# Kernel optimization log

Hardware: AMD Instinct MI355X
Metric: run time of the kernel (lower is better)

## Reference

```python
import jax, jax.numpy as jnp
import numpy as np

SEG = 4      # segment_size
H = 8        # n_heads
D = 1024     # d_model
B = 8
S = 4096


def setup_inputs() -> dict:
    key = jax.random.key(0)
    ks = jax.random.split(key, 9)
    s = 0.02  # init scale for weights
    return {
        "x": jax.random.normal(ks[0], (B, S, D), dtype=jnp.float32),
        "proj_qk_w": jax.random.normal(ks[1], (D, D), dtype=jnp.float32) * s,
        "proj_qk_b": jax.random.normal(ks[2], (D,), dtype=jnp.float32) * s,
        "proj_v_w": jax.random.normal(ks[3], (D, D), dtype=jnp.float32) * s,
        "proj_v_b": jax.random.normal(ks[4], (D,), dtype=jnp.float32) * s,
        "in_proj_w": jax.random.normal(ks[5], (3 * D, D), dtype=jnp.float32) * s,
        "in_proj_b": jax.random.normal(ks[6], (3 * D,), dtype=jnp.float32) * s,
        "out_proj_w": jax.random.normal(ks[7], (D, D), dtype=jnp.float32) * s,
        "out_proj_b": jax.random.normal(ks[8], (D,), dtype=jnp.float32) * s,
    }


def reference(x, proj_qk_w, proj_qk_b, proj_v_w, proj_v_b,
              in_proj_w, in_proj_b, out_proj_w, out_proj_b):
    b, seq_len, d = x.shape
    hd = d // H
    # torch: pad = seg - S % seg  (pads a full segment when S % seg == 0)
    pad = SEG - seq_len % SEG
    x = jnp.concatenate([x, x[:, :pad]], axis=1)          # [b, T, d]
    T = seq_len + pad
    a = T // SEG
    # cat(chunk(x, a, dim=1), dim=0): block-major stacking -> [a*b, SEG, d]
    xb = x.reshape(b, a, SEG, d).transpose(1, 0, 2, 3).reshape(a * b, SEG, d)

    # extra projections (same qk projection used for query and key)
    qk_in = xb @ proj_qk_w.T + proj_qk_b                   # [a*b, SEG, d]
    v_in = xb @ proj_v_w.T + proj_v_b

    # nn.MultiheadAttention in-projection
    wq, wk, wv = jnp.split(in_proj_w, 3, axis=0)
    bq, bk, bv = jnp.split(in_proj_b, 3)
    q = (qk_in @ wq.T + bq).reshape(a * b, SEG, H, hd)
    k = (qk_in @ wk.T + bk).reshape(a * b, SEG, H, hd)
    v = (v_in @ wv.T + bv).reshape(a * b, SEG, H, hd)

    scale = 1.0 / np.sqrt(hd).astype(np.float32)
    scores = jnp.einsum('nqhd,nkhd->nhqk', q * scale, k)   # [a*b, H, SEG, SEG]
    # diagonal exclusion mask (True on the diagonal = masked)
    diag = jnp.eye(SEG, dtype=bool)
    scores = jnp.where(diag[None, None], jnp.finfo(scores.dtype).min, scores)
    attn = jax.nn.softmax(scores, axis=-1)
    o = jnp.einsum('nhqk,nkhd->nqhd', attn, v).reshape(a * b, SEG, d)
    o = o @ out_proj_w.T + out_proj_b                      # [a*b, SEG, d]

    # cat(chunk(x, a, dim=0), dim=1): invert the block stacking
    out = o.reshape(a, b, SEG, d).transpose(1, 0, 2, 3).reshape(b, T, d)
    return out[:, :seq_len]
```

## Files before the change

### kernel.cpp

```cpp
#include <hip/hip_runtime.h>
#include <hip/hip_bf16.h>

typedef __bf16 bf16x8 __attribute__((ext_vector_type(8)));
typedef float f32x4 __attribute__((ext_vector_type(4)));

__device__ __forceinline__ float bf2f(unsigned int u) {
    unsigned int x = u << 16;
    return __builtin_bit_cast(float, x);
}
__device__ __forceinline__ unsigned short f2bf(float f) {
    unsigned int x = __builtin_bit_cast(unsigned int, f);
    x += 0x7fffu + ((x >> 16) & 1u);
    return (unsigned short)(x >> 16);
}

__device__ __forceinline__ void gld_lds16(const unsigned short* g, unsigned short* s) {
    __builtin_amdgcn_global_load_lds((const __attribute__((address_space(1))) void*)g,
                                     (__attribute__((address_space(3))) void*)s, 16, 0, 0);
}

template<bool OUT_F32>
__global__ __launch_bounds__(256) void gemm_bt(
    const unsigned short* __restrict__ A, int lda,
    const unsigned short* __restrict__ B,
    const unsigned short* __restrict__ B2, long bsplit,
    const float* __restrict__ bias,
    void* __restrict__ C, int N, int K)
{
    __shared__ unsigned short As[128 * 32];
    __shared__ unsigned short Bs[128 * 32];
    const int tid   = threadIdx.x;
    const int lane  = tid & 63;
    const int wave  = tid >> 6;
    const int wm    = (wave >> 1) * 64;
    const int wn    = (wave & 1) * 64;
    const int lrow  = lane & 15;
    const int lquad = lane >> 4;
    const long bm = (long)blockIdx.y * 128;
    const long bn = (long)blockIdx.x * 128;
    const unsigned short* Bp = (bm >= bsplit) ? B2 : B;

    f32x4 acc[4][4];
#pragma unroll
    for (int i = 0; i < 4; i++)
#pragma unroll
        for (int j = 0; j < 4; j++)
            acc[i][j] = (f32x4){0.f, 0.f, 0.f, 0.f};

    const int r0 = tid >> 2;
    const int c0 = (tid & 3) * 8;
    const unsigned short* Ag0 = A + (bm + r0) * (long)lda + c0;
    const unsigned short* Ag1 = A + (bm + r0 + 64) * (long)lda + c0;
    const unsigned short* Bg0 = Bp + (bn + r0) * (long)K + c0;
    const unsigned short* Bg1 = Bp + (bn + r0 + 64) * (long)K + c0;
    unsigned short* As0 = &As[tid * 8];
    unsigned short* As1 = &As[tid * 8 + 2048];
    unsigned short* Bs0 = &Bs[tid * 8];
    unsigned short* Bs1 = &Bs[tid * 8 + 2048];

    for (int k0 = 0; k0 < K; k0 += 32) {
        gld_lds16(Ag0 + k0, As0);
        gld_lds16(Ag1 + k0, As1);
        gld_lds16(Bg0 + k0, Bs0);
        gld_lds16(Bg1 + k0, Bs1);
        __syncthreads();
        bf16x8 af[4], bq[4];
#pragma unroll
        for (int i = 0; i < 4; i++)
            af[i] = *(const bf16x8*)&As[(wm + i * 16 + lrow) * 32 + lquad * 8];
#pragma unroll
        for (int j = 0; j < 4; j++)
            bq[j] = *(const bf16x8*)&Bs[(wn + j * 16 + lrow) * 32 + lquad * 8];
#pragma unroll
        for (int i = 0; i < 4; i++)
#pragma unroll
            for (int j = 0; j < 4; j++)
                acc[i][j] = __builtin_amdgcn_mfma_f32_16x16x32_bf16(bq[j], af[i], acc[i][j], 0, 0, 0);
        __syncthreads();
    }

#pragma unroll
    for (int i = 0; i < 4; i++) {
        const long row = bm + wm + i * 16 + lrow;
#pragma unroll
        for (int j = 0; j < 4; j++) {
            const int colb = (int)bn + wn + j * 16 + lquad * 4;
            float4 b4 = bias ? ((const float4*)bias)[colb >> 2]
                             : make_float4(0.f, 0.f, 0.f, 0.f);
            const float v0 = acc[i][j][0] + b4.x;
            const float v1 = acc[i][j][1] + b4.y;
            const float v2 = acc[i][j][2] + b4.z;
            const float v3 = acc[i][j][3] + b4.w;
            if (OUT_F32) {
                *(float4*)&((float*)C)[row * (long)N + colb] = make_float4(v0, v1, v2, v3);
            } else {
                unsigned int lo = (unsigned int)f2bf(v0) | ((unsigned int)f2bf(v1) << 16);
                unsigned int hi = (unsigned int)f2bf(v2) | ((unsigned int)f2bf(v3) << 16);
                *(uint2*)&((unsigned short*)C)[row * (long)N + colb] = make_uint2(lo, hi);
            }
        }
    }
}

__global__ __launch_bounds__(256) void attn4(
    const unsigned short* __restrict__ QKV,
    unsigned short* __restrict__ O)
{
    const int wave = threadIdx.x >> 6;
    const int lane = threadIdx.x & 63;
    const int half = lane >> 5;
    const int l    = lane & 31;
    const int gh = blockIdx.x * 8 + wave * 2 + half;
    const int g = gh >> 3, h = gh & 7;
    const long row0 = (long)g * 4;
    const int d0 = h * 128 + l * 4;
    const float scale = 0.08838834764831845f;

    float q[4][4], k[4][4], v[4][4];
#pragma unroll
    for (int i = 0; i < 4; i++) {
        const unsigned short* base = QKV + (row0 + i) * 3072 + d0;
        uint2 uq = *(const uint2*)base;
        uint2 uk = *(const uint2*)(base + 1024);
        uint2 uv = *(const uint2*)(base + 2048);
        q[i][0] = bf2f(uq.x & 0xffffu); q[i][1] = bf2f(uq.x >> 16);
        q[i][2] = bf2f(uq.y & 0xffffu); q[i][3] = bf2f(uq.y >> 16);
        k[i][0] = bf2f(uk.x & 0xffffu); k[i][1] = bf2f(uk.x >> 16);
        k[i][2] = bf2f(uk.y & 0xffffu); k[i][3] = bf2f(uk.y >> 16);
        v[i][0] = bf2f(uv.x & 0xffffu); v[i][1] = bf2f(uv.x >> 16);
        v[i][2] = bf2f(uv.y & 0xffffu); v[i][3] = bf2f(uv.y >> 16);
    }
    float s[4][4];
#pragma unroll
    for (int i = 0; i < 4; i++)
#pragma unroll
        for (int j = 0; j < 4; j++)
            s[i][j] = q[i][0] * k[j][0] + q[i][1] * k[j][1]
                    + q[i][2] * k[j][2] + q[i][3] * k[j][3];
#pragma unroll
    for (int m = 1; m < 32; m <<= 1)
#pragma unroll
        for (int i = 0; i < 4; i++)
#pragma unroll
            for (int j = 0; j < 4; j++)
                s[i][j] += __shfl_xor(s[i][j], m, 64);

#pragma unroll
    for (int i = 0; i < 4; i++) {
        float mx = -3.0e38f;
#pragma unroll
        for (int j = 0; j < 4; j++)
            if (j != i) mx = fmaxf(mx, s[i][j] * scale);
        float p[4], den = 0.f;
#pragma unroll
        for (int j = 0; j < 4; j++) {
            p[j] = (j == i) ? 0.f : __expf(s[i][j] * scale - mx);
            den += p[j];
        }
        const float inv = 1.f / den;
        float o0 = 0.f, o1 = 0.f, o2 = 0.f, o3 = 0.f;
#pragma unroll
        for (int j = 0; j < 4; j++) {
            const float a = p[j] * inv;
            o0 += a * v[j][0]; o1 += a * v[j][1];
            o2 += a * v[j][2]; o3 += a * v[j][3];
        }
        unsigned int lo = (unsigned int)f2bf(o0) | ((unsigned int)f2bf(o1) << 16);
        unsigned int hi = (unsigned int)f2bf(o2) | ((unsigned int)f2bf(o3) << 16);
        *(uint2*)(O + (row0 + i) * 1024 + d0) = make_uint2(lo, hi);
    }
}

__global__ __launch_bounds__(256) void cvt_bf16(const float* __restrict__ in,
                                                unsigned short* __restrict__ out, int n4)
{
    int i = blockIdx.x * blockDim.x + threadIdx.x;
    if (i >= n4) return;
    float4 v = ((const float4*)in)[i];
    unsigned int a = (unsigned int)f2bf(v.x) | ((unsigned int)f2bf(v.y) << 16);
    unsigned int b = (unsigned int)f2bf(v.z) | ((unsigned int)f2bf(v.w) << 16);
    ((uint2*)out)[i] = make_uint2(a, b);
}

__global__ __launch_bounds__(256) void cvt_weights(const float* __restrict__ win,
                                                   unsigned short* __restrict__ win16,
                                                   const float* __restrict__ wout,
                                                   unsigned short* __restrict__ wo16)
{
    int i = blockIdx.x * blockDim.x + threadIdx.x;
    const float* in;
    unsigned short* out;
    int j;
    if (i < 786432) { in = win; out = win16; j = i; }
    else            { in = wout; out = wo16; j = i - 786432; }
    float4 v = ((const float4*)in)[j];
    unsigned int a = (unsigned int)f2bf(v.x) | ((unsigned int)f2bf(v.y) << 16);
    unsigned int b = (unsigned int)f2bf(v.z) | ((unsigned int)f2bf(v.w) << 16);
    ((uint2*)out)[j] = make_uint2(a, b);
}

__global__ __launch_bounds__(256) void transpose_cvt2(const float* __restrict__ a,
                                                      unsigned short* __restrict__ oa,
                                                      const float* __restrict__ b,
                                                      unsigned short* __restrict__ ob, int n)
{
    const float* in = blockIdx.z ? b : a;
    unsigned short* out = blockIdx.z ? ob : oa;
    __shared__ unsigned short tile[64][65];
    const int bx = blockIdx.x * 64, by = blockIdx.y * 64;
    const int tx = threadIdx.x & 63, ty = threadIdx.x >> 6;
    for (int r = ty; r < 64; r += 4)
        tile[r][tx] = f2bf(in[(long)(by + r) * n + bx + tx]);
    __syncthreads();
    for (int r = ty; r < 64; r += 4)
        out[(long)(bx + r) * n + by + tx] = tile[tx][r];
}

__global__ __launch_bounds__(256) void bias_prep(const float* __restrict__ win,
                                                 const float* __restrict__ bqk,
                                                 const float* __restrict__ bv,
                                                 const float* __restrict__ bin,
                                                 float* __restrict__ bbig)
{
    const int row = blockIdx.x * 4 + (threadIdx.x >> 6);
    const int lane = threadIdx.x & 63;
    const float* b = (row < 2048) ? bqk : bv;
    float s = 0.f;
    for (int t = lane; t < 1024; t += 64) s += win[(long)row * 1024 + t] * b[t];
#pragma unroll
    for (int m = 1; m < 64; m <<= 1) s += __shfl_xor(s, m, 64);
    if (lane == 0) bbig[row] = s + bin[row];
}

extern "C" void kernel_launch(void* const* d_in, const int* in_sizes, int n_in,
                              void* d_out, int out_size, void* d_ws, size_t ws_size,
                              hipStream_t stream)
{
    (void)in_sizes; (void)n_in; (void)out_size; (void)ws_size;
    const float* x    = (const float*)d_in[0];
    const float* wqk  = (const float*)d_in[1];
    const float* bqk  = (const float*)d_in[2];
    const float* wv   = (const float*)d_in[3];
    const float* bv   = (const float*)d_in[4];
    const float* win  = (const float*)d_in[5];
    const float* bin  = (const float*)d_in[6];
    const float* wout = (const float*)d_in[7];
    const float* bout = (const float*)d_in[8];

    char* ws = (char*)d_ws;
    unsigned short* buf0  = (unsigned short*)ws;
    unsigned short* qkv   = (unsigned short*)(ws + (64ll << 20));
    unsigned short* win16 = (unsigned short*)(ws + (256ll << 20));
    unsigned short* wqkT  = (unsigned short*)(ws + (262ll << 20));
    unsigned short* wvT   = (unsigned short*)(ws + (264ll << 20));
    unsigned short* wbig  = (unsigned short*)(ws + (266ll << 20));
    unsigned short* wo16  = (unsigned short*)(ws + (272ll << 20));
    float*          bbig  = (float*)(ws + (274ll << 20));
    unsigned short* o16   = buf0;
    const long NOSPLIT = 1ll << 40;

    dim3 blk(256);
    cvt_bf16<<<32768, 256, 0, stream>>>(x, buf0, 8388608);
    cvt_weights<<<4096, 256, 0, stream>>>(win, win16, wout, wo16);
    transpose_cvt2<<<dim3(16, 16, 2), blk, 0, stream>>>(wqk, wqkT, wv, wvT, 1024);
    bias_prep<<<768, blk, 0, stream>>>(win, bqk, bv, bin, bbig);

    gemm_bt<false><<<dim3(8, 24), blk, 0, stream>>>(win16, 1024, wqkT, wvT, 2048,
                                                    nullptr, wbig, 1024, 1024);

    gemm_bt<false><<<dim3(24, 256), blk, 0, stream>>>(buf0, 1024, wbig, wbig, NOSPLIT,
                                                      bbig, qkv, 3072, 1024);

    attn4<<<8192, blk, 0, stream>>>(qkv, o16);

    gemm_bt<true><<<dim3(8, 256), blk, 0, stream>>>(o16, 1024, wo16, wo16, NOSPLIT,
                                                    bout, d_out, 1024, 1024);
}
```

Measured before the change: 735.5 us.

## Add 256x256 multi-stage pipelined GEMM for QKV and output projections

Introduces a 512-thread GEMM kernel with 256x256 tiles, a 4-slot LDS ring buffer that prefetches three k-steps ahead via direct global-to-LDS loads, and split A/B staging interleaved with MFMA phases under raised wave priority. Block indices are remapped so consecutive blocks are spread across XCD groups. The large QKV and output GEMMs move to this kernel to raise data reuse and hide load latency behind compute, in exchange for 128KB of LDS per block, more accumulator registers and lower occupancy.

```diff
diff --git a/kernel.cpp b/kernel.cpp
--- a/kernel.cpp
+++ b/kernel.cpp
@@ -20,67 +20,105 @@
 }
 
 template<bool OUT_F32>
-__global__ __launch_bounds__(256) void gemm_bt(
+__global__ __launch_bounds__(512) void gemm256(
     const unsigned short* __restrict__ A, int lda,
     const unsigned short* __restrict__ B,
-    const unsigned short* __restrict__ B2, long bsplit,
     const float* __restrict__ bias,
-    void* __restrict__ C, int N, int K)
-{
-    __shared__ unsigned short As[128 * 32];
-    __shared__ unsigned short Bs[128 * 32];
+    void* __restrict__ C, int N, int K, int nx)
+{
+    extern __shared__ char smem[];
     const int tid   = threadIdx.x;
     const int lane  = tid & 63;
     const int wave  = tid >> 6;
-    const int wm    = (wave >> 1) * 64;
-    const int wn    = (wave & 1) * 64;
+    const int wm    = (wave >> 2) * 128;
+    const int wn    = (wave & 3) * 64;
     const int lrow  = lane & 15;
     const int lquad = lane >> 4;
-    const long bm = (long)blockIdx.y * 128;
-    const long bn = (long)blockIdx.x * 128;
-    const unsigned short* Bp = (bm >= bsplit) ? B2 : B;
-
-    f32x4 acc[4][4];
-#pragma unroll
-    for (int i = 0; i < 4; i++)
+
+    int L = (int)blockIdx.x;
+    L = (L & 7) * ((int)gridDim.x >> 3) + (L >> 3);
+    const long bm = (long)(L / nx) * 256;
+    const long bn = (long)(L % nx) * 256;
+
+    const int srow = (lane & 7) + ((lane >> 5) << 3);
+    const int scol = ((lane >> 3) & 3) * 8;
+    const unsigned short* Asrc0 = A + (bm + wave * 16 + srow) * (long)lda + scol;
+    const unsigned short* Asrc1 = A + (bm + (8 + wave) * 16 + srow) * (long)lda + scol;
+    const unsigned short* Bsrc0 = B + (bn + wave * 16 + srow) * (long)K + scol;
+    const unsigned short* Bsrc1 = B + (bn + (8 + wave) * 16 + srow) * (long)K + scol;
+
+    const int dA0 = wave * 1024 + lane * 16;
+    const int dA1 = (8 + wave) * 1024 + lane * 16;
+    const int dB0 = 16384 + dA0;
+    const int dB1 = 16384 + dA1;
+
+    const int rdoff = (lrow & 7) * 16 + (lrow >> 3) * 512 + lquad * 128;
+
+    f32x4 acc[8][4];
+#pragma unroll
+    for (int i = 0; i < 8; i++)
 #pragma unroll
         for (int j = 0; j < 4; j++)
             acc[i][j] = (f32x4){0.f, 0.f, 0.f, 0.f};
 
-    const int r0 = tid >> 2;
-    const int c0 = (tid & 3) * 8;
-    const unsigned short* Ag0 = A + (bm + r0) * (long)lda + c0;
-    const unsigned short* Ag1 = A + (bm + r0 + 64) * (long)lda + c0;
-    const unsigned short* Bg0 = Bp + (bn + r0) * (long)K + c0;
-    const unsigned short* Bg1 = Bp + (bn + r0 + 64) * (long)K + c0;
-    unsigned short* As0 = &As[tid * 8];
-    unsigned short* As1 = &As[tid * 8 + 2048];
-    unsigned short* Bs0 = &Bs[tid * 8];
-    unsigned short* Bs1 = &Bs[tid * 8 + 2048];
-
-    for (int k0 = 0; k0 < K; k0 += 32) {
-        gld_lds16(Ag0 + k0, As0);
-        gld_lds16(Ag1 + k0, As1);
-        gld_lds16(Bg0 + k0, Bs0);
-        gld_lds16(Bg1 + k0, Bs1);
-        __syncthreads();
-        bf16x8 af[4], bq[4];
-#pragma unroll
-        for (int i = 0; i < 4; i++)
-            af[i] = *(const bf16x8*)&As[(wm + i * 16 + lrow) * 32 + lquad * 8];
-#pragma unroll
-        for (int j = 0; j < 4; j++)
-            bq[j] = *(const bf16x8*)&Bs[(wn + j * 16 + lrow) * 32 + lquad * 8];
+    const int NU = K >> 5;
+
+    auto stageA = [&](int su, int slot) {
+        char* sb = smem + (size_t)(slot * 32768);
+        gld_lds16(Asrc0 + su * 32, (unsigned short*)(sb + dA0));
+        gld_lds16(Asrc1 + su * 32, (unsigned short*)(sb + dA1));
+    };
+    auto stageB = [&](int su, int slot) {
+        char* sb = smem + (size_t)(slot * 32768);
+        gld_lds16(Bsrc0 + su * 32, (unsigned short*)(sb + dB0));
+        gld_lds16(Bsrc1 + su * 32, (unsigned short*)(sb + dB1));
+    };
+
+    stageA(0, 0); stageB(0, 0);
+    stageA(1, 1); stageB(1, 1);
+    stageA(2, 2); stageB(2, 2);
+    asm volatile("s_waitcnt vmcnt(8)\n\ts_barrier" ::: "memory");
+
+    for (int u = 0; u < NU; ++u) {
+        char* sl = smem + (size_t)((u & 3) * 32768);
+        const int us   = (u + 3 < NU) ? (u + 3) : (NU - 1);
+        const int slot = (u + 3) & 3;
+        bf16x8 af0[4], af1[4], bq[4];
+
+#pragma unroll
+        for (int j = 0; j < 4; j++)
+            bq[j] = *(const bf16x8*)(sl + 16384 + ((wn >> 4) + j) * 1024 + rdoff);
+#pragma unroll
+        for (int i = 0; i < 4; i++)
+            af0[i] = *(const bf16x8*)(sl + ((wm >> 4) + i) * 1024 + rdoff);
+        stageA(us, slot);
+        asm volatile("s_barrier" ::: "memory");
+        __builtin_amdgcn_s_setprio(1);
 #pragma unroll
         for (int i = 0; i < 4; i++)
 #pragma unroll
             for (int j = 0; j < 4; j++)
-                acc[i][j] = __builtin_amdgcn_mfma_f32_16x16x32_bf16(bq[j], af[i], acc[i][j], 0, 0, 0);
-        __syncthreads();
-    }
-
-#pragma unroll
-    for (int i = 0; i < 4; i++) {
+                acc[i][j] = __builtin_amdgcn_mfma_f32_16x16x32_bf16(bq[j], af0[i], acc[i][j], 0, 0, 0);
+        __builtin_amdgcn_s_setprio(0);
+        asm volatile("s_barrier" ::: "memory");
+
+#pragma unroll
+        for (int i = 0; i < 4; i++)
+            af1[i] = *(const bf16x8*)(sl + ((wm >> 4) + 4 + i) * 1024 + rdoff);
+        stageB(us, slot);
+        asm volatile("s_barrier" ::: "memory");
+        __builtin_amdgcn_s_setprio(1);
+#pragma unroll
+        for (int i = 0; i < 4; i++)
+#pragma unroll
+            for (int j = 0; j < 4; j++)
+                acc[4 + i][j] = __builtin_amdgcn_mfma_f32_16x16x32_bf16(bq[j], af1[i], acc[4 + i][j], 0, 0, 0);
+        __builtin_amdgcn_s_setprio(0);
+        asm volatile("s_waitcnt vmcnt(8)\n\ts_barrier" ::: "memory");
+    }
+
+#pragma unroll
+    for (int i = 0; i < 8; i++) {
         const long row = bm + wm + i * 16 + lrow;
 #pragma unroll
         for (int j = 0; j < 4; j++) {
@@ -102,6 +140,89 @@
     }
 }
 
+template<bool OUT_F32>
+__global__ __launch_bounds__(256) void gemm_bt(
+    const unsigned short* __restrict__ A, int lda,
+    const unsigned short* __restrict__ B,
+    const unsigned short* __restrict__ B2, long bsplit,
+    const float* __restrict__ bias,
+    void* __restrict__ C, int N, int K)
+{
+    __shared__ unsigned short As[128 * 32];
+    __shared__ unsigned short Bs[128 * 32];
+    const int tid   = threadIdx.x;
+    const int lane  = tid & 63;
+    const int wave  = tid >> 6;
+    const int wm    = (wave >> 1) * 64;
+    const int wn    = (wave & 1) * 64;
+    const int lrow  = lane & 15;
+    const int lquad = lane >> 4;
+    const long bm = (long)blockIdx.y * 128;
+    const long bn = (long)blockIdx.x * 128;
+    const unsigned short* Bp = (bm >= bsplit) ? B2 : B;
+
+    f32x4 acc[4][4];
+#pragma unroll
+    for (int i = 0; i < 4; i++)
+#pragma unroll
+        for (int j = 0; j < 4; j++)
+            acc[i][j] = (f32x4){0.f, 0.f, 0.f, 0.f};
+
+    const int r0 = tid >> 2;
+    const int c0 = (tid & 3) * 8;
+    const unsigned short* Ag0 = A + (bm + r0) * (long)lda + c0;
+    const unsigned short* Ag1 = A + (bm + r0 + 64) * (long)lda + c0;
+    const unsigned short* Bg0 = Bp + (bn + r0) * (long)K + c0;
+    const unsigned short* Bg1 = Bp + (bn + r0 + 64) * (long)K + c0;
+    unsigned short* As0 = &As[tid * 8];
+    unsigned short* As1 = &As[tid * 8 + 2048];
+    unsigned short* Bs0 = &Bs[tid * 8];
+    unsigned short* Bs1 = &Bs[tid * 8 + 2048];
+
+    for (int k0 = 0; k0 < K; k0 += 32) {
+        gld_lds16(Ag0 + k0, As0);
+        gld_lds16(Ag1 + k0, As1);
+        gld_lds16(Bg0 + k0, Bs0);
+        gld_lds16(Bg1 + k0, Bs1);
+        __syncthreads();
+        bf16x8 af[4], bq[4];
+#pragma unroll
+        for (int i = 0; i < 4; i++)
+            af[i] = *(const bf16x8*)&As[(wm + i * 16 + lrow) * 32 + lquad * 8];
+#pragma unroll
+        for (int j = 0; j < 4; j++)
+            bq[j] = *(const bf16x8*)&Bs[(wn + j * 16 + lrow) * 32 + lquad * 8];
+#pragma unroll
+        for (int i = 0; i < 4; i++)
+#pragma unroll
+            for (int j = 0; j < 4; j++)
+                acc[i][j] = __builtin_amdgcn_mfma_f32_16x16x32_bf16(bq[j], af[i], acc[i][j], 0, 0, 0);
+        __syncthreads();
+    }
+
+#pragma unroll
+    for (int i = 0; i < 4; i++) {
+        const long row = bm + wm + i * 16 + lrow;
+#pragma unroll
+        for (int j = 0; j < 4; j++) {
+            const int colb = (int)bn + wn + j * 16 + lquad * 4;
+            float4 b4 = bias ? ((const float4*)bias)[colb >> 2]
+                             : make_float4(0.f, 0.f, 0.f, 0.f);
+            const float v0 = acc[i][j][0] + b4.x;
+            const float v1 = acc[i][j][1] + b4.y;
+            const float v2 = acc[i][j][2] + b4.z;
+            const float v3 = acc[i][j][3] + b4.w;
+            if (OUT_F32) {
+                *(float4*)&((float*)C)[row * (long)N + colb] = make_float4(v0, v1, v2, v3);
+            } else {
+                unsigned int lo = (unsigned int)f2bf(v0) | ((unsigned int)f2bf(v1) << 16);
+                unsigned int hi = (unsigned int)f2bf(v2) | ((unsigned int)f2bf(v3) << 16);
+                *(uint2*)&((unsigned short*)C)[row * (long)N + colb] = make_uint2(lo, hi);
+            }
+        }
+    }
+}
+
 __global__ __launch_bounds__(256) void attn4(
     const unsigned short* __restrict__ QKV,
     unsigned short* __restrict__ O)
@@ -257,7 +378,11 @@
     unsigned short* wo16  = (unsigned short*)(ws + (272ll << 20));
     float*          bbig  = (float*)(ws + (274ll << 20));
     unsigned short* o16   = buf0;
-    const long NOSPLIT = 1ll << 40;
+
+    hipFuncSetAttribute(reinterpret_cast<const void*>(&gemm256<false>),
+                        hipFuncAttributeMaxDynamicSharedMemorySize, 131072);
+    hipFuncSetAttribute(reinterpret_cast<const void*>(&gemm256<true>),
+                        hipFuncAttributeMaxDynamicSharedMemorySize, 131072);
 
     dim3 blk(256);
     cvt_bf16<<<32768, 256, 0, stream>>>(x, buf0, 8388608);
@@ -268,11 +393,11 @@
     gemm_bt<false><<<dim3(8, 24), blk, 0, stream>>>(win16, 1024, wqkT, wvT, 2048,
                                                     nullptr, wbig, 1024, 1024);
 
-    gemm_bt<false><<<dim3(24, 256), blk, 0, stream>>>(buf0, 1024, wbig, wbig, NOSPLIT,
-                                                      bbig, qkv, 3072, 1024);
+    gemm256<false><<<dim3(12 * 128), 512, 131072, stream>>>(buf0, 1024, wbig,
+                                                            bbig, qkv, 3072, 1024, 12);
 
     attn4<<<8192, blk, 0, stream>>>(qkv, o16);
 
-    gemm_bt<true><<<dim3(8, 256), blk, 0, stream>>>(o16, 1024, wo16, wo16, NOSPLIT,
-                                                    bout, d_out, 1024, 1024);
-}
+    gemm256<true><<<dim3(4 * 128), 512, 131072, stream>>>(o16, 1024, wo16,
+                                                          bout, d_out, 1024, 1024, 4);
+}
```

Result: faster. 701.2 us (-4.7%).
